# Optimization experiments

Measured on AMD Instinct MI355X. Metric: run time of the kernel, lower is better.

## Reference

```python
import jax, jax.numpy as jnp
import numpy as np

V = 50000   # vocab_size
D = 128     # emb_dim
HID = 64    # hidden_dim
HEADS = 4   # gat_heads
N = 20000   # n_nodes
E = 320000  # n_edges
SLOPE = 0.2 # PyG GATConv leaky_relu negative_slope


def setup_inputs() -> dict:
    key = jax.random.key(0)
    ks = jax.random.split(key, 13)
    nrm = lambda k, shp: jax.random.normal(k, shp, jnp.float32) * 0.1
    return {
        "node_idxs": jax.random.randint(ks[0], (N,), 0, V),
        "edge_index": jax.random.randint(ks[1], (2, E), 0, N),
        "emb": nrm(ks[2], (V, D)),
        # GAT layer 1: in=D, out=HID per head, HEADS heads, concat
        "W1": nrm(ks[3], (D, HEADS * HID)),
        "att_src1": nrm(ks[4], (HEADS, HID)),
        "att_dst1": nrm(ks[5], (HEADS, HID)),
        "b1": jnp.zeros((HEADS * HID,), jnp.float32),
        # GAT layer 2: in=HEADS*HID, out=HID, 1 head
        "W2": nrm(ks[6], (HEADS * HID, HID)),
        "att_src2": nrm(ks[7], (1, HID)),
        "att_dst2": nrm(ks[8], (1, HID)),
        "b2": jnp.zeros((HID,), jnp.float32),
        # attentional pooling gate MLP: Linear(HID,HID) -> ReLU -> Linear(HID,1)
        "gate_W1": nrm(ks[9], (HID, HID)),
        "gate_b1": jnp.zeros((HID,), jnp.float32),
        "gate_W2": nrm(ks[10], (HID, 1)),
        "gate_b2": jnp.zeros((1,), jnp.float32),
    }


def _segment_softmax(logits, seg, num_segments):
    # numerically stable softmax over edges grouped by destination node
    m = jax.ops.segment_max(logits, seg, num_segments=num_segments)
    e = jnp.exp(logits - m[seg])
    s = jax.ops.segment_sum(e, seg, num_segments=num_segments)
    return e / s[seg]


def _gat_layer(x, src, dst, n, W, a_src, a_dst, b, heads, ch):
    h = (x @ W).reshape(n, heads, ch)                 # [N,H,C]
    alpha_src = jnp.einsum('nhc,hc->nh', h, a_src)    # [N,H]
    alpha_dst = jnp.einsum('nhc,hc->nh', h, a_dst)    # [N,H]
    logits = jax.nn.leaky_relu(alpha_src[src] + alpha_dst[dst], SLOPE)  # [E,H]
    alpha = _segment_softmax(logits, dst, n)          # [E,H]
    out = jax.ops.segment_sum(h[src] * alpha[..., None], dst, num_segments=n)  # [N,H,C]
    return out.reshape(n, heads * ch) + b


def reference(node_idxs, edge_index, emb, W1, att_src1, att_dst1, b1,
              W2, att_src2, att_dst2, b2, gate_W1, gate_b1, gate_W2, gate_b2):
    n = node_idxs.shape[0]
    # PyG GATConv default add_self_loops=True
    loops = jnp.arange(n)
    src = jnp.concatenate([edge_index[0], loops])
    dst = jnp.concatenate([edge_index[1], loops])

    x = emb[node_idxs]                                                  # [N,D]
    x = jax.nn.elu(_gat_layer(x, src, dst, n, W1, att_src1, att_dst1, b1, HEADS, HID))
    x = jax.nn.elu(_gat_layer(x, src, dst, n, W2, att_src2, att_dst2, b2, 1, HID))

    # AttentionalAggregation with index=zeros -> global softmax-gated pool
    gate = jax.nn.relu(x @ gate_W1 + gate_b1) @ gate_W2 + gate_b2       # [N,1]
    w = jax.nn.softmax(gate, axis=0)
    return jnp.sum(w * x, axis=0, keepdims=True)                        # [1,HID]
```

## Files before the change

kernel.cpp:

```cpp
#include <hip/hip_runtime.h>

typedef float v4 __attribute__((ext_vector_type(4)));

__device__ __forceinline__ float leaky(float x) { return x >= 0.f ? x : 0.2f * x; }
__device__ __forceinline__ float elu(float x) { return x > 0.f ? x : expm1f(x); }

__global__ void k_deg(const int* __restrict__ ei, int* __restrict__ deg, int nE, int eT) {
  int e = blockIdx.x * blockDim.x + threadIdx.x;
  if (e >= eT) return;
  int d = (e < nE) ? ei[nE + e] : (e - nE);
  atomicAdd(&deg[d], 1);
}

__global__ void k_scan(const int* __restrict__ deg, int* __restrict__ rowptr,
                       int* __restrict__ cursor, int nN, int eT) {
  __shared__ int sd[1024];
  int t = threadIdx.x;
  int chunk = (nN + 1023) >> 10;
  int beg = t * chunk;
  int end = beg + chunk; if (end > nN) end = nN;
  int s = 0;
  for (int i = beg; i < end; ++i) s += deg[i];
  sd[t] = s;
  __syncthreads();
  for (int off = 1; off < 1024; off <<= 1) {
    int v = (t >= off) ? sd[t - off] : 0;
    __syncthreads();
    sd[t] += v;
    __syncthreads();
  }
  int run = sd[t] - s;
  for (int i = beg; i < end; ++i) { rowptr[i] = run; cursor[i] = run; run += deg[i]; }
  if (t == 0) rowptr[nN] = eT;
}

__global__ void k_scatter(const int* __restrict__ ei, int* __restrict__ cursor,
                          int* __restrict__ srt, int nE, int eT) {
  int e = blockIdx.x * blockDim.x + threadIdx.x;
  if (e >= eT) return;
  int s, d;
  if (e < nE) { s = ei[e]; d = ei[nE + e]; } else { s = d = e - nE; }
  int pos = atomicAdd(&cursor[d], 1);
  srt[pos] = s;
}

__global__ __launch_bounds__(256) void k_gemm1(
    const int* __restrict__ nidx, const float* __restrict__ emb,
    const float* __restrict__ W1, const float* __restrict__ asv,
    const float* __restrict__ adv, float* __restrict__ h1,
    float* __restrict__ as1, float* __restrict__ ad1, int nN) {
  __shared__ __align__(16) float xs[64 * 68];
  __shared__ __align__(16) float Ws[64 * 64];
  int t = threadIdx.x;
  int nbase = (blockIdx.x >> 2) * 64;
  int head  = blockIdx.x & 3;
  int cbase = head * 64;
  int c0 = (t & 15) * 4;
  int n0 = (t >> 4) * 4;
  float acc[4][4];
  for (int i = 0; i < 4; ++i) for (int j = 0; j < 4; ++j) acc[i][j] = 0.f;
  v4 z = (v4)(0.f);
  for (int kc = 0; kc < 2; ++kc) {
    __syncthreads();
    {
      int sn = t >> 2;
      int node = nbase + sn;
      int kp = (t & 3) * 16;
      bool v = node < nN;
      const float* sp = &emb[(size_t)nidx[v ? node : nN - 1] * 128 + kc * 64 + kp];
      v4 a0 = v ? *(const v4*)(sp + 0)  : z;
      v4 a1 = v ? *(const v4*)(sp + 4)  : z;
      v4 a2 = v ? *(const v4*)(sp + 8)  : z;
      v4 a3 = v ? *(const v4*)(sp + 12) : z;
      *(v4*)&xs[sn * 68 + kp + 0]  = a0;
      *(v4*)&xs[sn * 68 + kp + 4]  = a1;
      *(v4*)&xs[sn * 68 + kp + 8]  = a2;
      *(v4*)&xs[sn * 68 + kp + 12] = a3;
    }
    {
      int kk = t >> 2;
      int cp = (t & 3) * 16;
      const float* wp = &W1[(size_t)(kc * 64 + kk) * 256 + cbase + cp];
      v4 w0 = *(const v4*)(wp + 0);
      v4 w1 = *(const v4*)(wp + 4);
      v4 w2 = *(const v4*)(wp + 8);
      v4 w3 = *(const v4*)(wp + 12);
      *(v4*)&Ws[kk * 64 + cp + 0]  = w0;
      *(v4*)&Ws[kk * 64 + cp + 4]  = w1;
      *(v4*)&Ws[kk * 64 + cp + 8]  = w2;
      *(v4*)&Ws[kk * 64 + cp + 12] = w3;
    }
    __syncthreads();
    #pragma unroll 4
    for (int kk = 0; kk < 64; kk += 4) {
      v4 xv[4], wv[4];
      for (int i = 0; i < 4; ++i) xv[i] = *(const v4*)&xs[(n0 + i) * 68 + kk];
      for (int j = 0; j < 4; ++j) wv[j] = *(const v4*)&Ws[(kk + j) * 64 + c0];
      for (int i = 0; i < 4; ++i)
        for (int j = 0; j < 4; ++j) {
          float xd = xv[i][j];
          acc[i][0] += xd * wv[j][0];
          acc[i][1] += xd * wv[j][1];
          acc[i][2] += xd * wv[j][2];
          acc[i][3] += xd * wv[j][3];
        }
    }
  }
  v4 asl = *(const v4*)&asv[cbase + c0];
  v4 adl = *(const v4*)&adv[cbase + c0];
  for (int i = 0; i < 4; ++i) {
    int node = nbase + n0 + i;
    v4 o; o[0] = acc[i][0]; o[1] = acc[i][1]; o[2] = acc[i][2]; o[3] = acc[i][3];
    float ps = o[0]*asl[0] + o[1]*asl[1] + o[2]*asl[2] + o[3]*asl[3];
    float pd = o[0]*adl[0] + o[1]*adl[1] + o[2]*adl[2] + o[3]*adl[3];
    ps += __shfl_xor(ps, 1); pd += __shfl_xor(pd, 1);
    ps += __shfl_xor(ps, 2); pd += __shfl_xor(pd, 2);
    ps += __shfl_xor(ps, 4); pd += __shfl_xor(pd, 4);
    ps += __shfl_xor(ps, 8); pd += __shfl_xor(pd, 8);
    if (node < nN) {
      *(v4*)&h1[(size_t)node * 256 + cbase + c0] = o;
      if ((t & 15) == 0) {
        as1[(size_t)node * 4 + head] = ps;
        ad1[(size_t)node * 4 + head] = pd;
      }
    }
  }
}

__global__ __launch_bounds__(256) void k_agg1(
    const float* __restrict__ h1, const float* __restrict__ as1,
    const float* __restrict__ ad1, const float* __restrict__ b1,
    const int* __restrict__ rowptr, const int* __restrict__ srt,
    float* __restrict__ x2, int nN) {
  __shared__ int   ss[4][64];
  __shared__ float sw[4][256];
  int t = threadIdx.x;
  int wv = t >> 6, lane = t & 63;
  int n = blockIdx.x * 4 + wv;
  if (n >= nN) return;
  int ms0 = rowptr[n], ms1 = rowptr[n + 1];
  v4 adn = *(const v4*)&ad1[(size_t)n * 4];
  int h = lane >> 4;
  v4 acc = (v4)(0.f);
  float den = 0.f;
  for (int base = ms0; base < ms1; base += 64) {
    int m = ms1 - base; if (m > 64) m = 64;
    asm volatile("s_waitcnt lgkmcnt(0)" ::: "memory");
    __builtin_amdgcn_wave_barrier();
    if (lane < m) {
      int s = srt[base + lane];
      ss[wv][lane] = s;
      v4 a = *(const v4*)&as1[(size_t)s * 4];
      sw[wv][lane * 4 + 0] = __expf(leaky(a[0] + adn[0]));
      sw[wv][lane * 4 + 1] = __expf(leaky(a[1] + adn[1]));
      sw[wv][lane * 4 + 2] = __expf(leaky(a[2] + adn[2]));
      sw[wv][lane * 4 + 3] = __expf(leaky(a[3] + adn[3]));
    }
    asm volatile("s_waitcnt lgkmcnt(0)" ::: "memory");
    __builtin_amdgcn_wave_barrier();
    #pragma unroll 8
    for (int j = 0; j < m; ++j) {
      int s = ss[wv][j];
      float wj = sw[wv][j * 4 + h];
      v4 hv = *(const v4*)&h1[(size_t)s * 256 + lane * 4];
      acc[0] += wj * hv[0];
      acc[1] += wj * hv[1];
      acc[2] += wj * hv[2];
      acc[3] += wj * hv[3];
      den += wj;
    }
  }
  v4 bb = *(const v4*)&b1[lane * 4];
  float inv = 1.f / den;
  v4 o;
  o[0] = elu(acc[0] * inv + bb[0]);
  o[1] = elu(acc[1] * inv + bb[1]);
  o[2] = elu(acc[2] * inv + bb[2]);
  o[3] = elu(acc[3] * inv + bb[3]);
  *(v4*)&x2[(size_t)n * 256 + lane * 4] = o;
}

__global__ __launch_bounds__(256) void k_gemm2(
    const float* __restrict__ x2, const float* __restrict__ W2,
    const float* __restrict__ asv, const float* __restrict__ adv,
    float* __restrict__ h2, float* __restrict__ as2, float* __restrict__ ad2, int nN) {
  __shared__ __align__(16) float xs[32 * 68];
  __shared__ __align__(16) float Ws[64 * 64];
  int t = threadIdx.x;
  int nbase = blockIdx.x * 32;
  int c0 = (t & 15) * 4;
  int n0 = (t >> 4) * 2;
  float acc[2][4];
  for (int i = 0; i < 2; ++i) for (int j = 0; j < 4; ++j) acc[i][j] = 0.f;
  v4 z = (v4)(0.f);
  for (int kc = 0; kc < 4; ++kc) {
    __syncthreads();
    {
      int sn = t >> 3;
      int node = nbase + sn;
      int kp = (t & 7) * 8;
      bool v = node < nN;
      const float* sp = &x2[(size_t)(v ? node : nN - 1) * 256 + kc * 64 + kp];
      v4 a0 = v ? *(const v4*)(sp + 0) : z;
      v4 a1 = v ? *(const v4*)(sp + 4) : z;
      *(v4*)&xs[sn * 68 + kp + 0] = a0;
      *(v4*)&xs[sn * 68 + kp + 4] = a1;
    }
    {
      int kk = t >> 2;
      int cp = (t & 3) * 16;
      const float* wp = &W2[(size_t)(kc * 64 + kk) * 64 + cp];
      v4 w0 = *(const v4*)(wp + 0);
      v4 w1 = *(const v4*)(wp + 4);
      v4 w2 = *(const v4*)(wp + 8);
      v4 w3 = *(const v4*)(wp + 12);
      *(v4*)&Ws[kk * 64 + cp + 0]  = w0;
      *(v4*)&Ws[kk * 64 + cp + 4]  = w1;
      *(v4*)&Ws[kk * 64 + cp + 8]  = w2;
      *(v4*)&Ws[kk * 64 + cp + 12] = w3;
    }
    __syncthreads();
    #pragma unroll 4
    for (int kk = 0; kk < 64; kk += 4) {
      v4 xv[2], wv[4];
      for (int i = 0; i < 2; ++i) xv[i] = *(const v4*)&xs[(n0 + i) * 68 + kk];
      for (int j = 0; j < 4; ++j) wv[j] = *(const v4*)&Ws[(kk + j) * 64 + c0];
      for (int i = 0; i < 2; ++i)
        for (int j = 0; j < 4; ++j) {
          float xd = xv[i][j];
          acc[i][0] += xd * wv[j][0];
          acc[i][1] += xd * wv[j][1];
          acc[i][2] += xd * wv[j][2];
          acc[i][3] += xd * wv[j][3];
        }
    }
  }
  v4 asl = *(const v4*)&asv[c0];
  v4 adl = *(const v4*)&adv[c0];
  for (int i = 0; i < 2; ++i) {
    int node = nbase + n0 + i;
    v4 o; o[0] = acc[i][0]; o[1] = acc[i][1]; o[2] = acc[i][2]; o[3] = acc[i][3];
    float ps = o[0]*asl[0] + o[1]*asl[1] + o[2]*asl[2] + o[3]*asl[3];
    float pd = o[0]*adl[0] + o[1]*adl[1] + o[2]*adl[2] + o[3]*adl[3];
    ps += __shfl_xor(ps, 1); pd += __shfl_xor(pd, 1);
    ps += __shfl_xor(ps, 2); pd += __shfl_xor(pd, 2);
    ps += __shfl_xor(ps, 4); pd += __shfl_xor(pd, 4);
    ps += __shfl_xor(ps, 8); pd += __shfl_xor(pd, 8);
    if (node < nN) {
      *(v4*)&h2[(size_t)node * 64 + c0] = o;
      if ((t & 15) == 0) { as2[node] = ps; ad2[node] = pd; }
    }
  }
}

__global__ __launch_bounds__(256) void k_agg2(
    const float* __restrict__ h2, const float* __restrict__ as2,
    const float* __restrict__ ad2, const float* __restrict__ b2,
    const int* __restrict__ rowptr, const int* __restrict__ srt,
    float* __restrict__ x3, int nN) {
  __shared__ int   ss[4][64];
  __shared__ float sw[4][64];
  int t = threadIdx.x;
  int wv = t >> 6, lane = t & 63;
  int n = blockIdx.x * 4 + wv;
  if (n >= nN) return;
  int ms0 = rowptr[n], ms1 = rowptr[n + 1];
  float adn = ad2[n];
  float acc = 0.f, den = 0.f;
  for (int base = ms0; base < ms1; base += 64) {
    int m = ms1 - base; if (m > 64) m = 64;
    asm volatile("s_waitcnt lgkmcnt(0)" ::: "memory");
    __builtin_amdgcn_wave_barrier();
    if (lane < m) {
      int s = srt[base + lane];
      ss[wv][lane] = s;
      sw[wv][lane] = __expf(leaky(as2[s] + adn));
    }
    asm volatile("s_waitcnt lgkmcnt(0)" ::: "memory");
    __builtin_amdgcn_wave_barrier();
    #pragma unroll 8
    for (int j = 0; j < m; ++j) {
      int s = ss[wv][j];
      float wj = sw[wv][j];
      acc += wj * h2[(size_t)s * 64 + lane];
      den += wj;
    }
  }
  x3[(size_t)n * 64 + lane] = elu(acc / den + b2[lane]);
}

__global__ __launch_bounds__(512) void k_gatepool(
    const float* __restrict__ x3, const float* __restrict__ gW1,
    const float* __restrict__ gb1, const float* __restrict__ gW2,
    const float* __restrict__ gb2, float* __restrict__ pnum,
    float* __restrict__ pden, int nN) {
  __shared__ __align__(16) float gwT[64 * 68];
  __shared__ float xr[8][64];
  __shared__ float snum[8][64];
  __shared__ float sden[8];
  int t = threadIdx.x;
  int wv = t >> 6, lane = t & 63;
  for (int i = t; i < 4096; i += 512) {
    int d = i >> 6, c = i & 63;
    gwT[c * 68 + d] = gW1[i];
  }
  float gb1l = gb1[lane];
  float gw2l = gW2[lane];
  float gb2s = gb2[0];
  __syncthreads();
  float num = 0.f, den = 0.f;
  int nIt = (nN + 2047) >> 11;
  int off0 = blockIdx.x * 8 + wv;
  for (int it = 0; it < nIt; ++it) {
    int n = off0 + it * 2048;
    bool v = n < nN;
    float xv = v ? x3[(size_t)n * 64 + lane] : 0.f;
    xr[wv][lane] = xv;
    asm volatile("s_waitcnt lgkmcnt(0)" ::: "memory");
    __builtin_amdgcn_wave_barrier();
    float hid = gb1l;
    for (int d4 = 0; d4 < 64; d4 += 4) {
      v4 xs4 = *(const v4*)&xr[wv][d4];
      v4 gv  = *(const v4*)&gwT[lane * 68 + d4];
      hid += xs4[0] * gv[0] + xs4[1] * gv[1] + xs4[2] * gv[2] + xs4[3] * gv[3];
    }
    hid = fmaxf(hid, 0.f);
    float p = hid * gw2l;
    for (int o = 32; o; o >>= 1) p += __shfl_xor(p, o);
    float g = __expf(p + gb2s);
    if (v) { num += g * xv; den += g; }
    asm volatile("s_waitcnt lgkmcnt(0)" ::: "memory");
    __builtin_amdgcn_wave_barrier();
  }
  snum[wv][lane] = num;
  if (lane == 0) sden[wv] = den;
  __syncthreads();
  if (t < 64) {
    float s = 0.f;
    for (int k = 0; k < 8; ++k) s += snum[k][t];
    pnum[blockIdx.x * 64 + t] = s;
  }
  if (t == 0) {
    float s = 0.f;
    for (int k = 0; k < 8; ++k) s += sden[k];
    pden[blockIdx.x] = s;
  }
}

__global__ void k_final(const float* __restrict__ pnum, const float* __restrict__ pden,
                        float* __restrict__ out) {
  int t = threadIdx.x;
  float s = 0.f, dn = 0.f;
  for (int b = 0; b < 256; ++b) { s += pnum[b * 64 + t]; dn += pden[b]; }
  out[t] = s / dn;
}

extern "C" void kernel_launch(void* const* d_in, const int* in_sizes, int n_in,
                              void* d_out, int out_size, void* d_ws, size_t ws_size,
                              hipStream_t stream) {
  const int*   nidx = (const int*)d_in[0];
  const int*   ei   = (const int*)d_in[1];
  const float* emb  = (const float*)d_in[2];
  const float* W1   = (const float*)d_in[3];
  const float* as1v = (const float*)d_in[4];
  const float* ad1v = (const float*)d_in[5];
  const float* b1   = (const float*)d_in[6];
  const float* W2   = (const float*)d_in[7];
  const float* as2v = (const float*)d_in[8];
  const float* ad2v = (const float*)d_in[9];
  const float* b2   = (const float*)d_in[10];
  const float* gW1  = (const float*)d_in[11];
  const float* gb1  = (const float*)d_in[12];
  const float* gW2  = (const float*)d_in[13];
  const float* gb2  = (const float*)d_in[14];
  float* out = (float*)d_out;

  const int nN = in_sizes[0];
  const int nE = in_sizes[1] / 2;
  const int eT = nE + nN;

  float* f = (float*)d_ws;
  size_t off = 0;
  float* h1   = f + off; off += (size_t)nN * 256;
  float* x2   = f + off; off += (size_t)nN * 256;
  float* as1  = f + off; off += (size_t)nN * 4;
  float* ad1  = f + off; off += (size_t)nN * 4;
  float* as2  = f + off; off += nN;
  float* ad2  = f + off; off += nN;
  float* pnum = f + off; off += 256 * 64;
  float* pden = f + off; off += 256;
  int* deg    = (int*)(f + off); off += nN;
  int* rowptr = (int*)(f + off); off += nN + 1;
  int* cursor = (int*)(f + off); off += nN;
  int* srt    = (int*)(f + off); off += eT;

  float* h2 = h1;
  float* x3 = h1 + (size_t)nN * 128;

  hipMemsetAsync(deg, 0, (size_t)nN * sizeof(int), stream);

  int eb = (eT + 255) / 256;
  k_deg    <<<eb, 256, 0, stream>>>(ei, deg, nE, eT);
  k_scan   <<<1, 1024, 0, stream>>>(deg, rowptr, cursor, nN, eT);
  k_scatter<<<eb, 256, 0, stream>>>(ei, cursor, srt, nE, eT);

  int nt64 = (nN + 63) / 64;
  k_gemm1 <<<nt64 * 4, 256, 0, stream>>>(nidx, emb, W1, as1v, ad1v, h1, as1, ad1, nN);
  k_agg1  <<<(nN + 3) / 4, 256, 0, stream>>>(h1, as1, ad1, b1, rowptr, srt, x2, nN);

  k_gemm2 <<<(nN + 31) / 32, 256, 0, stream>>>(x2, W2, as2v, ad2v, h2, as2, ad2, nN);
  k_agg2  <<<(nN + 3) / 4, 256, 0, stream>>>(h2, as2, ad2, b2, rowptr, srt, x3, nN);

  k_gatepool<<<256, 512, 0, stream>>>(x3, gW1, gb1, gW2, gb2, pnum, pden, nN);
  k_final   <<<1, 64, 0, stream>>>(pnum, pden, out);
}
```

Measured before the change: 290.9 us.

## Aggregate raw embeddings before layer-1 projection and widen agg2 lane mapping

Layer 1 is reordered using linearity: the attention logits come from precomputed W1·att vectors, and the raw 128-dim embeddings are softmax-aggregated per head before the GEMM with W1. Each edge gather then reads 128 floats instead of the 256-float projected rows, at the cost of a 512-wide intermediate per node and two extra small kernels. Separately, agg2 now processes four edges per iteration using v4 loads and cross-lane shuffles to finish the reduction, which means fewer serial loop steps per node.

```diff
diff --git a/kernel.cpp b/kernel.cpp
--- a/kernel.cpp
+++ b/kernel.cpp
@@ -1,6 +1,7 @@
 #include <hip/hip_runtime.h>
 
 typedef float v4 __attribute__((ext_vector_type(4)));
+typedef float v2 __attribute__((ext_vector_type(2)));
 
 __device__ __forceinline__ float leaky(float x) { return x >= 0.f ? x : 0.2f * x; }
 __device__ __forceinline__ float elu(float x) { return x > 0.f ? x : expm1f(x); }
@@ -44,11 +45,102 @@
   srt[pos] = s;
 }
 
-__global__ __launch_bounds__(256) void k_gemm1(
+__global__ __launch_bounds__(256) void k_prep(const float* __restrict__ W1,
+                                              const float* __restrict__ asv,
+                                              const float* __restrict__ adv,
+                                              float* __restrict__ uv) {
+  int i = blockIdx.x * 256 + threadIdx.x;
+  if (i >= 512) return;
+  int k = i >> 2, h = i & 3;
+  const float* w = &W1[(size_t)k * 256 + h * 64];
+  const float* a = &asv[h * 64];
+  const float* d = &adv[h * 64];
+  float su = 0.f, sv = 0.f;
+  #pragma unroll 8
+  for (int c = 0; c < 64; ++c) { float x = w[c]; su += x * a[c]; sv += x * d[c]; }
+  uv[k * 8 + h]     = su;
+  uv[k * 8 + 4 + h] = sv;
+}
+
+__global__ __launch_bounds__(256) void k_attn1(
     const int* __restrict__ nidx, const float* __restrict__ emb,
-    const float* __restrict__ W1, const float* __restrict__ asv,
-    const float* __restrict__ adv, float* __restrict__ h1,
-    float* __restrict__ as1, float* __restrict__ ad1, int nN) {
+    const float* __restrict__ uv, float* __restrict__ as1,
+    float* __restrict__ ad1, int nN) {
+  int t = threadIdx.x;
+  int wv = t >> 6, lane = t & 63;
+  int n = blockIdx.x * 4 + wv;
+  if (n >= nN) return;
+  const float* xp = &emb[(size_t)nidx[n] * 128];
+  v2 x = *(const v2*)&xp[lane * 2];
+  v4 u0 = *(const v4*)&uv[(lane * 2) * 8];
+  v4 d0 = *(const v4*)&uv[(lane * 2) * 8 + 4];
+  v4 u1 = *(const v4*)&uv[(lane * 2 + 1) * 8];
+  v4 d1 = *(const v4*)&uv[(lane * 2 + 1) * 8 + 4];
+  v4 ps = u0 * x[0] + u1 * x[1];
+  v4 pd = d0 * x[0] + d1 * x[1];
+  for (int o = 32; o; o >>= 1) {
+    ps[0] += __shfl_xor(ps[0], o); ps[1] += __shfl_xor(ps[1], o);
+    ps[2] += __shfl_xor(ps[2], o); ps[3] += __shfl_xor(ps[3], o);
+    pd[0] += __shfl_xor(pd[0], o); pd[1] += __shfl_xor(pd[1], o);
+    pd[2] += __shfl_xor(pd[2], o); pd[3] += __shfl_xor(pd[3], o);
+  }
+  if (lane == 0) {
+    *(v4*)&as1[(size_t)n * 4] = ps;
+    *(v4*)&ad1[(size_t)n * 4] = pd;
+  }
+}
+
+__global__ __launch_bounds__(256) void k_aggx(
+    const int* __restrict__ nidx, const float* __restrict__ emb,
+    const float* __restrict__ as1, const float* __restrict__ ad1,
+    const int* __restrict__ rowptr, const int* __restrict__ srt,
+    float* __restrict__ g, int nN) {
+  __shared__ int   ss[4][64];
+  __shared__ float sw[4][256];
+  int t = threadIdx.x;
+  int wv = t >> 6, lane = t & 63;
+  int n = blockIdx.x * 4 + wv;
+  if (n >= nN) return;
+  int ms0 = rowptr[n], ms1 = rowptr[n + 1];
+  v4 adn = *(const v4*)&ad1[(size_t)n * 4];
+  v2 acc0 = (v2)(0.f), acc1 = (v2)(0.f), acc2 = (v2)(0.f), acc3 = (v2)(0.f);
+  float den0 = 0.f, den1 = 0.f, den2 = 0.f, den3 = 0.f;
+  for (int base = ms0; base < ms1; base += 64) {
+    int m = ms1 - base; if (m > 64) m = 64;
+    asm volatile("s_waitcnt lgkmcnt(0)" ::: "memory");
+    __builtin_amdgcn_wave_barrier();
+    if (lane < m) {
+      int s = srt[base + lane];
+      ss[wv][lane] = nidx[s];
+      v4 a = *(const v4*)&as1[(size_t)s * 4];
+      sw[wv][lane * 4 + 0] = __expf(leaky(a[0] + adn[0]));
+      sw[wv][lane * 4 + 1] = __expf(leaky(a[1] + adn[1]));
+      sw[wv][lane * 4 + 2] = __expf(leaky(a[2] + adn[2]));
+      sw[wv][lane * 4 + 3] = __expf(leaky(a[3] + adn[3]));
+    }
+    asm volatile("s_waitcnt lgkmcnt(0)" ::: "memory");
+    __builtin_amdgcn_wave_barrier();
+    #pragma unroll 8
+    for (int j = 0; j < m; ++j) {
+      int r = ss[wv][j];
+      v4 w = *(const v4*)&sw[wv][j * 4];
+      v2 xv = *(const v2*)&emb[(size_t)r * 128 + lane * 2];
+      acc0 += w[0] * xv; den0 += w[0];
+      acc1 += w[1] * xv; den1 += w[1];
+      acc2 += w[2] * xv; den2 += w[2];
+      acc3 += w[3] * xv; den3 += w[3];
+    }
+  }
+  size_t gb = (size_t)n * 512 + lane * 2;
+  *(v2*)&g[gb + 0]   = acc0 * (1.f / den0);
+  *(v2*)&g[gb + 128] = acc1 * (1.f / den1);
+  *(v2*)&g[gb + 256] = acc2 * (1.f / den2);
+  *(v2*)&g[gb + 384] = acc3 * (1.f / den3);
+}
+
+__global__ __launch_bounds__(256) void k_gemm1b(
+    const float* __restrict__ g, const float* __restrict__ W1,
+    const float* __restrict__ b1, float* __restrict__ x2, int nN) {
   __shared__ __align__(16) float xs[64 * 68];
   __shared__ __align__(16) float Ws[64 * 64];
   int t = threadIdx.x;
@@ -67,7 +159,7 @@
       int node = nbase + sn;
       int kp = (t & 3) * 16;
       bool v = node < nN;
-      const float* sp = &emb[(size_t)nidx[v ? node : nN - 1] * 128 + kc * 64 + kp];
+      const float* sp = &g[(size_t)(v ? node : nN - 1) * 512 + head * 128 + kc * 64 + kp];
       v4 a0 = v ? *(const v4*)(sp + 0)  : z;
       v4 a1 = v ? *(const v4*)(sp + 4)  : z;
       v4 a2 = v ? *(const v4*)(sp + 8)  : z;
@@ -106,78 +198,18 @@
         }
     }
   }
-  v4 asl = *(const v4*)&asv[cbase + c0];
-  v4 adl = *(const v4*)&adv[cbase + c0];
+  v4 bb = *(const v4*)&b1[cbase + c0];
   for (int i = 0; i < 4; ++i) {
     int node = nbase + n0 + i;
-    v4 o; o[0] = acc[i][0]; o[1] = acc[i][1]; o[2] = acc[i][2]; o[3] = acc[i][3];
-    float ps = o[0]*asl[0] + o[1]*asl[1] + o[2]*asl[2] + o[3]*asl[3];
-    float pd = o[0]*adl[0] + o[1]*adl[1] + o[2]*adl[2] + o[3]*adl[3];
-    ps += __shfl_xor(ps, 1); pd += __shfl_xor(pd, 1);
-    ps += __shfl_xor(ps, 2); pd += __shfl_xor(pd, 2);
-    ps += __shfl_xor(ps, 4); pd += __shfl_xor(pd, 4);
-    ps += __shfl_xor(ps, 8); pd += __shfl_xor(pd, 8);
     if (node < nN) {
-      *(v4*)&h1[(size_t)node * 256 + cbase + c0] = o;
-      if ((t & 15) == 0) {
-        as1[(size_t)node * 4 + head] = ps;
-        ad1[(size_t)node * 4 + head] = pd;
-      }
-    }
-  }
-}
-
-__global__ __launch_bounds__(256) void k_agg1(
-    const float* __restrict__ h1, const float* __restrict__ as1,
-    const float* __restrict__ ad1, const float* __restrict__ b1,
-    const int* __restrict__ rowptr, const int* __restrict__ srt,
-    float* __restrict__ x2, int nN) {
-  __shared__ int   ss[4][64];
-  __shared__ float sw[4][256];
-  int t = threadIdx.x;
-  int wv = t >> 6, lane = t & 63;
-  int n = blockIdx.x * 4 + wv;
-  if (n >= nN) return;
-  int ms0 = rowptr[n], ms1 = rowptr[n + 1];
-  v4 adn = *(const v4*)&ad1[(size_t)n * 4];
-  int h = lane >> 4;
-  v4 acc = (v4)(0.f);
-  float den = 0.f;
-  for (int base = ms0; base < ms1; base += 64) {
-    int m = ms1 - base; if (m > 64) m = 64;
-    asm volatile("s_waitcnt lgkmcnt(0)" ::: "memory");
-    __builtin_amdgcn_wave_barrier();
-    if (lane < m) {
-      int s = srt[base + lane];
-      ss[wv][lane] = s;
-      v4 a = *(const v4*)&as1[(size_t)s * 4];
-      sw[wv][lane * 4 + 0] = __expf(leaky(a[0] + adn[0]));
-      sw[wv][lane * 4 + 1] = __expf(leaky(a[1] + adn[1]));
-      sw[wv][lane * 4 + 2] = __expf(leaky(a[2] + adn[2]));
-      sw[wv][lane * 4 + 3] = __expf(leaky(a[3] + adn[3]));
-    }
-    asm volatile("s_waitcnt lgkmcnt(0)" ::: "memory");
-    __builtin_amdgcn_wave_barrier();
-    #pragma unroll 8
-    for (int j = 0; j < m; ++j) {
-      int s = ss[wv][j];
-      float wj = sw[wv][j * 4 + h];
-      v4 hv = *(const v4*)&h1[(size_t)s * 256 + lane * 4];
-      acc[0] += wj * hv[0];
-      acc[1] += wj * hv[1];
-      acc[2] += wj * hv[2];
-      acc[3] += wj * hv[3];
-      den += wj;
-    }
-  }
-  v4 bb = *(const v4*)&b1[lane * 4];
-  float inv = 1.f / den;
-  v4 o;
-  o[0] = elu(acc[0] * inv + bb[0]);
-  o[1] = elu(acc[1] * inv + bb[1]);
-  o[2] = elu(acc[2] * inv + bb[2]);
-  o[3] = elu(acc[3] * inv + bb[3]);
-  *(v4*)&x2[(size_t)n * 256 + lane * 4] = o;
+      v4 o;
+      o[0] = elu(acc[i][0] + bb[0]);
+      o[1] = elu(acc[i][1] + bb[1]);
+      o[2] = elu(acc[i][2] + bb[2]);
+      o[3] = elu(acc[i][3] + bb[3]);
+      *(v4*)&x2[(size_t)node * 256 + cbase + c0] = o;
+    }
+  }
 }
 
 __global__ __launch_bounds__(256) void k_gemm2(
@@ -266,27 +298,48 @@
   if (n >= nN) return;
   int ms0 = rowptr[n], ms1 = rowptr[n + 1];
   float adn = ad2[n];
-  float acc = 0.f, den = 0.f;
+  int grp = lane >> 4;
+  int c4  = (lane & 15) * 4;
+  v4 acc = (v4)(0.f);
+  float den = 0.f;
   for (int base = ms0; base < ms1; base += 64) {
     int m = ms1 - base; if (m > 64) m = 64;
     asm volatile("s_waitcnt lgkmcnt(0)" ::: "memory");
     __builtin_amdgcn_wave_barrier();
-    if (lane < m) {
-      int s = srt[base + lane];
+    {
+      int s = 0; float ww = 0.f;
+      if (lane < m) { s = srt[base + lane]; ww = __expf(leaky(as2[s] + adn)); }
       ss[wv][lane] = s;
-      sw[wv][lane] = __expf(leaky(as2[s] + adn));
-    }
-    asm volatile("s_waitcnt lgkmcnt(0)" ::: "memory");
-    __builtin_amdgcn_wave_barrier();
-    #pragma unroll 8
-    for (int j = 0; j < m; ++j) {
-      int s = ss[wv][j];
-      float wj = sw[wv][j];
-      acc += wj * h2[(size_t)s * 64 + lane];
+      sw[wv][lane] = ww;
+    }
+    asm volatile("s_waitcnt lgkmcnt(0)" ::: "memory");
+    __builtin_amdgcn_wave_barrier();
+    int mq = (m + 3) & ~3;
+    #pragma unroll 4
+    for (int j = 0; j < mq; j += 4) {
+      int s = ss[wv][j + grp];
+      float wj = sw[wv][j + grp];
+      v4 hv = *(const v4*)&h2[(size_t)s * 64 + c4];
+      acc += wj * hv;
       den += wj;
     }
   }
-  x3[(size_t)n * 64 + lane] = elu(acc / den + b2[lane]);
+  acc[0] += __shfl_xor(acc[0], 16); acc[1] += __shfl_xor(acc[1], 16);
+  acc[2] += __shfl_xor(acc[2], 16); acc[3] += __shfl_xor(acc[3], 16);
+  den += __shfl_xor(den, 16);
+  acc[0] += __shfl_xor(acc[0], 32); acc[1] += __shfl_xor(acc[1], 32);
+  acc[2] += __shfl_xor(acc[2], 32); acc[3] += __shfl_xor(acc[3], 32);
+  den += __shfl_xor(den, 32);
+  if (lane < 16) {
+    float inv = 1.f / den;
+    v4 bb = *(const v4*)&b2[c4];
+    v4 o;
+    o[0] = elu(acc[0] * inv + bb[0]);
+    o[1] = elu(acc[1] * inv + bb[1]);
+    o[2] = elu(acc[2] * inv + bb[2]);
+    o[3] = elu(acc[3] * inv + bb[3]);
+    *(v4*)&x3[(size_t)n * 64 + c4] = o;
+  }
 }
 
 __global__ __launch_bounds__(512) void k_gatepool(
@@ -381,12 +434,13 @@
 
   float* f = (float*)d_ws;
   size_t off = 0;
-  float* h1   = f + off; off += (size_t)nN * 256;
+  float* g    = f + off; off += (size_t)nN * 512;
   float* x2   = f + off; off += (size_t)nN * 256;
   float* as1  = f + off; off += (size_t)nN * 4;
   float* ad1  = f + off; off += (size_t)nN * 4;
   float* as2  = f + off; off += nN;
   float* ad2  = f + off; off += nN;
+  float* uv   = f + off; off += 1024;
   float* pnum = f + off; off += 256 * 64;
   float* pden = f + off; off += 256;
   int* deg    = (int*)(f + off); off += nN;
@@ -394,8 +448,8 @@
   int* cursor = (int*)(f + off); off += nN;
   int* srt    = (int*)(f + off); off += eT;
 
-  float* h2 = h1;
-  float* x3 = h1 + (size_t)nN * 128;
+  float* h2 = g;
+  float* x3 = g + (size_t)nN * 64;
 
   hipMemsetAsync(deg, 0, (size_t)nN * sizeof(int), stream);
 
@@ -404,9 +458,12 @@
   k_scan   <<<1, 1024, 0, stream>>>(deg, rowptr, cursor, nN, eT);
   k_scatter<<<eb, 256, 0, stream>>>(ei, cursor, srt, nE, eT);
 
+  k_prep  <<<2, 256, 0, stream>>>(W1, as1v, ad1v, uv);
+  k_attn1 <<<(nN + 3) / 4, 256, 0, stream>>>(nidx, emb, uv, as1, ad1, nN);
+  k_aggx  <<<(nN + 3) / 4, 256, 0, stream>>>(nidx, emb, as1, ad1, rowptr, srt, g, nN);
+
   int nt64 = (nN + 63) / 64;
-  k_gemm1 <<<nt64 * 4, 256, 0, stream>>>(nidx, emb, W1, as1v, ad1v, h1, as1, ad1, nN);
-  k_agg1  <<<(nN + 3) / 4, 256, 0, stream>>>(h1, as1, ad1, b1, rowptr, srt, x2, nN);
+  k_gemm1b<<<nt64 * 4, 256, 0, stream>>>(g, W1, b1, x2, nN);
 
   k_gemm2 <<<(nN + 31) / 32, 256, 0, stream>>>(x2, W2, as2v, ad2v, h2, as2, ad2, nN);
   k_agg2  <<<(nN + 3) / 4, 256, 0, stream>>>(h2, as2, ad2, b2, rowptr, srt, x3, nN);
```

Measured after the change: 299.5 us. 1.03x slower.
